# Kernel optimization log

Measured on AMD Instinct MI355X. Metric: run time of the kernel, lower is better.

## Reference

```python
import jax, jax.numpy as jnp
import numpy as np


def _gcn_norm(edge_index, num_nodes, dtype):
    # PyG GCNConv.norm: add self-loops (weight 1), symmetric deg^{-1/2} normalization
    row, col = edge_index[0], edge_index[1]
    loop = jnp.arange(num_nodes, dtype=row.dtype)
    row = jnp.concatenate([row, loop])
    col = jnp.concatenate([col, loop])
    ew = jnp.ones(row.shape[0], dtype=dtype)
    deg = jax.ops.segment_sum(ew, row, num_segments=num_nodes)
    dis = jnp.where(deg > 0, jax.lax.rsqrt(deg), 0.0)
    norm = dis[row] * ew * dis[col]
    return row, col, norm


def _masked_gcn_conv(x, row, col, norm, sigma, W, b, num_nodes):
    # mask_features: edge gather -> diff/sigma -> square -> scatter-add -> exp mask
    h = (x[col] - x[row]) / sigma            # [E, F]
    h = norm[:, None] * h * h                # [E, F]
    mask = jax.ops.segment_sum(h, row, num_segments=num_nodes)        # [N, F]
    deg = jax.ops.segment_sum(jnp.ones_like(norm), row, num_segments=num_nodes)  # degree(source), >=1 due to self-loops
    x = x * jnp.exp(-mask / deg[:, None])
    # GCNConv: linear transform then normalized aggregation source->target
    xw = x @ W                               # [N, O]
    out = jax.ops.segment_sum(norm[:, None] * xw[row], col, num_segments=num_nodes)
    return out + b


def setup_inputs() -> dict:
    key = jax.random.key(0)
    ks = jax.random.split(key, 8)
    N, E, F, H, C = 100000, 1600000, 128, 64, 40
    g = 1.414  # xavier gain used for sigma
    return {
        "x": jax.random.normal(ks[0], (N, F), jnp.float32),
        "edge_index": jax.random.randint(ks[1], (2, E), 0, N, jnp.int64),
        "sigma1": jax.random.uniform(ks[2], (1, F), jnp.float32, -1.0, 1.0) * (g * np.sqrt(6.0 / (1 + F))),
        "W1": jax.random.normal(ks[3], (F, H), jnp.float32) * (1.0 / np.sqrt(F)),
        "b1": jnp.zeros((H,), jnp.float32),
        "sigma2": jax.random.uniform(ks[4], (1, H), jnp.float32, -1.0, 1.0) * (g * np.sqrt(6.0 / (1 + H))),
        "W2": jax.random.normal(ks[5], (H, C), jnp.float32) * (1.0 / np.sqrt(H)),
        "b2": jnp.zeros((C,), jnp.float32),
    }


def reference(x, edge_index, sigma1, W1, b1, sigma2, W2, b2):
    N = x.shape[0]
    row, col, norm = _gcn_norm(edge_index, N, x.dtype)
    x = _masked_gcn_conv(x, row, col, norm, sigma1, W1, b1, N)
    x = jax.nn.relu(x)
    # dropout is identity in eval mode
    x = _masked_gcn_conv(x, row, col, norm, sigma2, W2, b2, N)
    return jax.nn.log_softmax(x, axis=1)
```

## Files before the change

kernel.cpp:

```cpp
#include <hip/hip_runtime.h>
#include <cmath>

constexpr int F1 = 128;
constexpr int H  = 64;
constexpr int NC = 40;
constexpr int NPART = 4;

constexpr int SCAN_TPB = 256;
constexpr int SCAN_IPT = 8;
constexpr int SCAN_EPB = SCAN_TPB * SCAN_IPT;

__device__ inline unsigned short f2bf(float f) {
    union { float f; unsigned u; } v; v.f = f;
    return (unsigned short)((v.u + 0x7FFFu + ((v.u >> 16) & 1u)) >> 16);
}
__device__ inline float bflo(unsigned p) { union { float f; unsigned u; } v; v.u = p << 16; return v.f; }
__device__ inline float bfhi(unsigned p) { union { float f; unsigned u; } v; v.u = p & 0xFFFF0000u; return v.f; }
__device__ inline void unpack8(uint4 raw, float* d) {
    d[0] = bflo(raw.x); d[1] = bfhi(raw.x); d[2] = bflo(raw.y); d[3] = bfhi(raw.y);
    d[4] = bflo(raw.z); d[5] = bfhi(raw.z); d[6] = bflo(raw.w); d[7] = bfhi(raw.w);
}

__global__ void isg_kernel(const float* __restrict__ s1, float* __restrict__ i1,
                           const float* __restrict__ s2, float* __restrict__ i2) {
    int i = threadIdx.x;
    if (i < F1) i1[i] = 1.0f / s1[i];
    if (i < H)  i2[i] = 1.0f / s2[i];
}

__global__ void count8_prep_kernel(const int* __restrict__ row, const int* __restrict__ col,
                                   int* __restrict__ cntO, int* __restrict__ cntI,
                                   int E, int chunk, int stride, int cntBlocks,
                                   const float* __restrict__ x, const float* __restrict__ isg,
                                   unsigned short* __restrict__ u, size_t n8) {
    int bid = blockIdx.x;
    if (bid < cntBlocks) {
        int p = bid & (NPART - 1);
        int gid = bid / NPART;
        unsigned lo = (unsigned)(p * chunk);
        for (int e = gid * blockDim.x + threadIdx.x; e < E; e += stride) {
            int r = row[e], c = col[e];
            if ((unsigned)r - lo < (unsigned)chunk) atomicAdd(&cntO[r], 1);
            if ((unsigned)c - lo < (unsigned)chunk) atomicAdd(&cntI[c], 1);
        }
    } else {
        size_t idx = (size_t)(bid - cntBlocks) * blockDim.x + threadIdx.x;
        if (idx >= n8) return;
        size_t base = idx * 8;
        int fk = (int)(base % (size_t)F1);
        float4 a0 = *(const float4*)&x[base];
        float4 a1 = *(const float4*)&x[base + 4];
        float4 s0 = *(const float4*)&isg[fk];
        float4 s1 = *(const float4*)&isg[fk + 4];
        uint4 p4;
        p4.x = (unsigned)f2bf(a0.x * s0.x) | ((unsigned)f2bf(a0.y * s0.y) << 16);
        p4.y = (unsigned)f2bf(a0.z * s0.z) | ((unsigned)f2bf(a0.w * s0.w) << 16);
        p4.z = (unsigned)f2bf(a1.x * s1.x) | ((unsigned)f2bf(a1.y * s1.y) << 16);
        p4.w = (unsigned)f2bf(a1.z * s1.z) | ((unsigned)f2bf(a1.w * s1.w) << 16);
        *(uint4*)&u[base] = p4;
    }
}

__global__ void scan_partial_kernel(const int* __restrict__ cnt, int* __restrict__ bsum, int M) {
    __shared__ int red[SCAN_TPB];
    int t = threadIdx.x;
    int i0 = blockIdx.x * SCAN_EPB + t * SCAN_IPT;
    int s = 0;
#pragma unroll
    for (int k = 0; k < SCAN_IPT; ++k) {
        int i = i0 + k;
        if (i < M) s += cnt[i];
    }
    red[t] = s;
    __syncthreads();
    for (int off = SCAN_TPB / 2; off > 0; off >>= 1) {
        if (t < off) red[t] += red[t + off];
        __syncthreads();
    }
    if (t == 0) bsum[blockIdx.x] = red[0];
}

__global__ void scan_offsets_kernel(int* __restrict__ bsum, int nb,
                                    int* __restrict__ rowptrO, int* __restrict__ rowptrI,
                                    int N, int E) {
    __shared__ int sh[1024];
    int t = threadIdx.x;
    sh[t] = (t < nb) ? bsum[t] : 0;
    __syncthreads();
    for (int off = 1; off < 1024; off <<= 1) {
        int v = (t >= off) ? sh[t - off] : 0;
        __syncthreads();
        sh[t] += v;
        __syncthreads();
    }
    if (t < nb) bsum[t] = (t > 0) ? sh[t - 1] : 0;
    if (t == 0) { rowptrO[N] = E; rowptrI[N] = E; }
}

__global__ void scan_final_kernel(int* __restrict__ cntO, int* __restrict__ cntI,
                                  const int* __restrict__ bsum,
                                  int* __restrict__ rowptrO, int* __restrict__ rowptrI,
                                  float* __restrict__ dis, int N, int E) {
    __shared__ int sh[SCAN_TPB];
    int t = threadIdx.x;
    int M = 2 * N;
    const int* cnt = cntO;
    int i0 = blockIdx.x * SCAN_EPB + t * SCAN_IPT;
    int cv[SCAN_IPT], pre[SCAN_IPT];
    int run = 0;
#pragma unroll
    for (int k = 0; k < SCAN_IPT; ++k) {
        int i = i0 + k;
        cv[k] = (i < M) ? cnt[i] : 0;
        pre[k] = run;
        run += cv[k];
    }
    sh[t] = run;
    __syncthreads();
    for (int off = 1; off < SCAN_TPB; off <<= 1) {
        int v = (t >= off) ? sh[t - off] : 0;
        __syncthreads();
        sh[t] += v;
        __syncthreads();
    }
    int toff = ((t > 0) ? sh[t - 1] : 0) + bsum[blockIdx.x];
#pragma unroll
    for (int k = 0; k < SCAN_IPT; ++k) {
        int i = i0 + k;
        if (i < M) {
            int val = toff + pre[k];
            if (i < N) {
                rowptrO[i] = val;
                cntO[i] = val;
                dis[i] = rsqrtf((float)(cv[k] + 1));
            } else {
                rowptrI[i - N] = val - E;
                cntI[i - N] = val - E;
            }
        }
    }
}

__global__ void build8_kernel(const int* __restrict__ row, const int* __restrict__ col,
                              int* __restrict__ curO, int* __restrict__ curI,
                              int2* __restrict__ adjO2, int2* __restrict__ adjI2,
                              const float* __restrict__ dis,
                              int E, int chunk, int stride) {
    int p = blockIdx.x & (NPART - 1);
    int gid = blockIdx.x / NPART;
    unsigned lo = (unsigned)(p * chunk);
    for (int e = gid * blockDim.x + threadIdx.x; e < E; e += stride) {
        int r = row[e], c = col[e];
        bool inR = (unsigned)r - lo < (unsigned)chunk;
        bool inC = (unsigned)c - lo < (unsigned)chunk;
        if (inR | inC) {
            float nrm = dis[r] * dis[c];
            int nb = __float_as_int(nrm);
            if (inR) adjO2[atomicAdd(&curO[r], 1)] = make_int2(c, nb);
            if (inC) adjI2[atomicAdd(&curI[c], 1)] = make_int2(r, nb);
        }
    }
}

template<int F, int O, int R>
__global__ void fused_mask_gemm_kernel(const int* __restrict__ rowptr, const int2* __restrict__ adj2,
                                       const float* __restrict__ sig,
                                       const unsigned short* __restrict__ u,
                                       const float* __restrict__ W,
                                       unsigned short* __restrict__ Ybf, int N) {
    constexpr int NT = R * 64;
    constexpr int G = F / 8;
    constexpr int NPI = 64 / G;
    __shared__ __align__(16) float Ws[F * O];
    __shared__ __align__(16) float Xs[R][F];
    int tid = threadIdx.x;
    for (int i = tid; i < F * O; i += NT) Ws[i] = W[i];
    int w = tid >> 6, lane = tid & 63;
    int h = lane / G, j = lane % G;
    int r = blockIdx.x * R + w;
    if (r < N) {
        int beg = rowptr[r], end = rowptr[r + 1];
        float inv_deg = 1.0f / (float)(end - beg + 1);
        float ur[8], acc[8];
        unpack8(*(const uint4*)&u[(size_t)r * F + 8 * j], ur);
#pragma unroll
        for (int k = 0; k < 8; ++k) acc[k] = 0.0f;
        for (int t = beg; t < end; t += 2 * NPI) {
            int e0 = t + h, e1 = t + NPI + h;
            int2 a0 = adj2[min(e0, end - 1)];
            int2 a1 = adj2[min(e1, end - 1)];
            float n0 = (e0 < end) ? __int_as_float(a0.y) : 0.0f;
            float n1 = (e1 < end) ? __int_as_float(a1.y) : 0.0f;
            uint4 rw0 = *(const uint4*)&u[(size_t)a0.x * F + 8 * j];
            uint4 rw1 = *(const uint4*)&u[(size_t)a1.x * F + 8 * j];
            float uc[8];
            unpack8(rw0, uc);
#pragma unroll
            for (int q = 0; q < 8; ++q) {
                float d = uc[q] - ur[q];
                acc[q] = fmaf(n0 * d, d, acc[q]);
            }
            unpack8(rw1, uc);
#pragma unroll
            for (int q = 0; q < 8; ++q) {
                float d = uc[q] - ur[q];
                acc[q] = fmaf(n1 * d, d, acc[q]);
            }
        }
#pragma unroll
        for (int off = G; off < 64; off <<= 1) {
#pragma unroll
            for (int k = 0; k < 8; ++k) acc[k] += __shfl_xor(acc[k], off);
        }
        if (h == 0) {
            float4 s0 = *(const float4*)&sig[8 * j];
            float4 s1 = *(const float4*)&sig[8 * j + 4];
            float sg[8] = {s0.x, s0.y, s0.z, s0.w, s1.x, s1.y, s1.z, s1.w};
            float xm[8];
#pragma unroll
            for (int k = 0; k < 8; ++k) xm[k] = ur[k] * sg[k] * expf(-acc[k] * inv_deg);
            *(float4*)&Xs[w][8 * j]     = make_float4(xm[0], xm[1], xm[2], xm[3]);
            *(float4*)&Xs[w][8 * j + 4] = make_float4(xm[4], xm[5], xm[6], xm[7]);
        }
    }
    __syncthreads();
    if (r < N && lane < O) {
        float acc = 0.0f;
#pragma unroll
        for (int fq = 0; fq < F / 4; ++fq) {
            float4 xs = *(const float4*)&Xs[w][4 * fq];
            acc = fmaf(xs.x, Ws[(4 * fq + 0) * O + lane], acc);
            acc = fmaf(xs.y, Ws[(4 * fq + 1) * O + lane], acc);
            acc = fmaf(xs.z, Ws[(4 * fq + 2) * O + lane], acc);
            acc = fmaf(xs.w, Ws[(4 * fq + 3) * O + lane], acc);
        }
        float other = __shfl_xor(acc, 1);
        if (!(lane & 1)) {
            *(unsigned*)&Ybf[(size_t)r * O + lane] =
                (unsigned)f2bf(acc) | ((unsigned)f2bf(other) << 16);
        }
    }
}

__global__ void agg_relu_kernel(const int* __restrict__ rowptr, const int2* __restrict__ adj2,
                                const float* __restrict__ dis, const unsigned short* __restrict__ ybf,
                                const float* __restrict__ bias,
                                unsigned short* __restrict__ u2, const float* __restrict__ isg2, int N) {
    int c = blockIdx.x * (blockDim.x >> 6) + (threadIdx.x >> 6);
    if (c >= N) return;
    int lane = threadIdx.x & 63;
    int h = lane >> 3, j = lane & 7;
    int beg = rowptr[c], end = rowptr[c + 1];
    float acc[8];
#pragma unroll
    for (int k = 0; k < 8; ++k) acc[k] = 0.0f;
    for (int t = beg; t < end; t += 16) {
        int e0 = t + h, e1 = t + 8 + h;
        int2 a0 = adj2[min(e0, end - 1)];
        int2 a1 = adj2[min(e1, end - 1)];
        float n0 = (e0 < end) ? __int_as_float(a0.y) : 0.0f;
        float n1 = (e1 < end) ? __int_as_float(a1.y) : 0.0f;
        uint4 rw0 = *(const uint4*)&ybf[(size_t)a0.x * H + 8 * j];
        uint4 rw1 = *(const uint4*)&ybf[(size_t)a1.x * H + 8 * j];
        float v[8];
        unpack8(rw0, v);
#pragma unroll
        for (int q = 0; q < 8; ++q) acc[q] = fmaf(n0, v[q], acc[q]);
        unpack8(rw1, v);
#pragma unroll
        for (int q = 0; q < 8; ++q) acc[q] = fmaf(n1, v[q], acc[q]);
    }
#pragma unroll
    for (int off = 8; off < 64; off <<= 1) {
#pragma unroll
        for (int k = 0; k < 8; ++k) acc[k] += __shfl_xor(acc[k], off);
    }
    if (h == 0) {
        float dc = dis[c];
        float sv[8];
        unpack8(*(const uint4*)&ybf[(size_t)c * H + 8 * j], sv);
        float4 b0 = *(const float4*)&bias[8 * j];
        float4 b1v = *(const float4*)&bias[8 * j + 4];
        float bb[8] = {b0.x, b0.y, b0.z, b0.w, b1v.x, b1v.y, b1v.z, b1v.w};
        float4 s0 = *(const float4*)&isg2[8 * j];
        float4 s1 = *(const float4*)&isg2[8 * j + 4];
        float sg[8] = {s0.x, s0.y, s0.z, s0.w, s1.x, s1.y, s1.z, s1.w};
        float hv[8];
        float d2 = dc * dc;
#pragma unroll
        for (int k = 0; k < 8; ++k) hv[k] = fmaxf(fmaf(d2, sv[k], acc[k]) + bb[k], 0.0f);
        uint4 p;
        p.x = (unsigned)f2bf(hv[0] * sg[0]) | ((unsigned)f2bf(hv[1] * sg[1]) << 16);
        p.y = (unsigned)f2bf(hv[2] * sg[2]) | ((unsigned)f2bf(hv[3] * sg[3]) << 16);
        p.z = (unsigned)f2bf(hv[4] * sg[4]) | ((unsigned)f2bf(hv[5] * sg[5]) << 16);
        p.w = (unsigned)f2bf(hv[6] * sg[6]) | ((unsigned)f2bf(hv[7] * sg[7]) << 16);
        *(uint4*)&u2[(size_t)c * H + 8 * j] = p;
    }
}

__global__ void agg_lsm_kernel(const int* __restrict__ rowptr, const int2* __restrict__ adj2,
                               const float* __restrict__ dis, const unsigned short* __restrict__ ybf,
                               const float* __restrict__ bias, float* __restrict__ out, int N) {
    int c = blockIdx.x * (blockDim.x >> 6) + (threadIdx.x >> 6);
    if (c >= N) return;
    int lane = threadIdx.x & 63;
    int h = lane >> 4, j = lane & 15;
    bool active = j < 10;
    int beg = rowptr[c], end = rowptr[c + 1];
    float a[4] = {0.f, 0.f, 0.f, 0.f};
    for (int t = beg; t < end; t += 8) {
        int e0 = t + h, e1 = t + 4 + h;
        int2 a0 = adj2[min(e0, end - 1)];
        int2 a1 = adj2[min(e1, end - 1)];
        float n0 = (e0 < end) ? __int_as_float(a0.y) : 0.0f;
        float n1 = (e1 < end) ? __int_as_float(a1.y) : 0.0f;
        uint2 rw0 = active ? *(const uint2*)&ybf[(size_t)a0.x * NC + 4 * j] : make_uint2(0u, 0u);
        uint2 rw1 = active ? *(const uint2*)&ybf[(size_t)a1.x * NC + 4 * j] : make_uint2(0u, 0u);
        a[0] = fmaf(n0, bflo(rw0.x), a[0]); a[1] = fmaf(n0, bfhi(rw0.x), a[1]);
        a[2] = fmaf(n0, bflo(rw0.y), a[2]); a[3] = fmaf(n0, bfhi(rw0.y), a[3]);
        a[0] = fmaf(n1, bflo(rw1.x), a[0]); a[1] = fmaf(n1, bfhi(rw1.x), a[1]);
        a[2] = fmaf(n1, bflo(rw1.y), a[2]); a[3] = fmaf(n1, bfhi(rw1.y), a[3]);
    }
#pragma unroll
    for (int off = 16; off < 64; off <<= 1) {
#pragma unroll
        for (int k = 0; k < 4; ++k) a[k] += __shfl_xor(a[k], off);
    }
    bool wr = (h == 0) && active;
    float v[4] = {-INFINITY, -INFINITY, -INFINITY, -INFINITY};
    if (wr) {
        float dc = dis[c];
        uint2 sr = *(const uint2*)&ybf[(size_t)c * NC + 4 * j];
        float sv[4] = {bflo(sr.x), bfhi(sr.x), bflo(sr.y), bfhi(sr.y)};
        float4 bb = *(const float4*)&bias[4 * j];
        float b4[4] = {bb.x, bb.y, bb.z, bb.w};
        float d2 = dc * dc;
#pragma unroll
        for (int k = 0; k < 4; ++k) v[k] = fmaf(d2, sv[k], a[k]) + b4[k];
    }
    float m = fmaxf(fmaxf(v[0], v[1]), fmaxf(v[2], v[3]));
#pragma unroll
    for (int off = 8; off > 0; off >>= 1) m = fmaxf(m, __shfl_xor(m, off));
    float s = wr ? (expf(v[0] - m) + expf(v[1] - m) + expf(v[2] - m) + expf(v[3] - m)) : 0.0f;
#pragma unroll
    for (int off = 8; off > 0; off >>= 1) s += __shfl_xor(s, off);
    float mls = m + logf(s);
    if (wr)
        *(float4*)&out[(size_t)c * NC + 4 * j] = make_float4(v[0] - mls, v[1] - mls, v[2] - mls, v[3] - mls);
}

extern "C" void kernel_launch(void* const* d_in, const int* in_sizes, int n_in,
                              void* d_out, int out_size, void* d_ws, size_t ws_size,
                              hipStream_t stream) {
    const float* x    = (const float*)d_in[0];
    const int*   ei   = (const int*)  d_in[1];
    const float* sig1 = (const float*)d_in[2];
    const float* W1   = (const float*)d_in[3];
    const float* b1   = (const float*)d_in[4];
    const float* sig2 = (const float*)d_in[5];
    const float* W2   = (const float*)d_in[6];
    const float* b2   = (const float*)d_in[7];
    float* out = (float*)d_out;

    const int N = in_sizes[0] / F1;
    const int E = in_sizes[1] / 2;
    const int* row = ei;
    const int* col = ei + E;

    char* w = (char*)d_ws;
    auto alloc = [&](size_t bytes) { void* q = w; w += (bytes + 255) & ~255ull; return q; };
    int*   cntO    = (int*)  alloc((size_t)2 * N * 4);
    int*   cntI    = cntO + N;
    int*   rowptrO = (int*)  alloc((size_t)(N + 1) * 4);
    int*   rowptrI = (int*)  alloc((size_t)(N + 1) * 4);
    int2*  adjO2   = (int2*) alloc((size_t)E * 8);
    int2*  adjI2   = (int2*) alloc((size_t)E * 8);
    float* dis     = (float*)alloc((size_t)N * 4);
    float* isg1    = (float*)alloc(F1 * 4);
    float* isg2    = (float*)alloc(H * 4);
    int*   bsum    = (int*)  alloc(1024 * 4);
    unsigned short* u1   = (unsigned short*)alloc((size_t)N * F1 * 2);
    unsigned short* u2   = (unsigned short*)alloc((size_t)N * H * 2);
    unsigned short* ybf1 = (unsigned short*)alloc((size_t)N * H * 2);
    unsigned short* ybf2 = u1;

    const int B = 256;
    const int chunk = (N + NPART - 1) / NPART;
    const int TOTB = 8192;
    const int stride4 = (TOTB / NPART) * B;
    const size_t n8 = (size_t)N * F1 / 8;
    const int prepBlocks = (int)((n8 + B - 1) / B);
    const int M = 2 * N;
    const int nb = (M + SCAN_EPB - 1) / SCAN_EPB;

    hipMemsetAsync(cntO, 0, (size_t)2 * N * 4, stream);
    isg_kernel<<<1, 128, 0, stream>>>(sig1, isg1, sig2, isg2);
    count8_prep_kernel<<<TOTB + prepBlocks, B, 0, stream>>>(
        row, col, cntO, cntI, E, chunk, stride4, TOTB, x, isg1, u1, n8);
    scan_partial_kernel<<<nb, SCAN_TPB, 0, stream>>>(cntO, bsum, M);
    scan_offsets_kernel<<<1, 1024, 0, stream>>>(bsum, nb, rowptrO, rowptrI, N, E);
    scan_final_kernel<<<nb, SCAN_TPB, 0, stream>>>(cntO, cntI, bsum, rowptrO, rowptrI, dis, N, E);
    build8_kernel<<<TOTB, B, 0, stream>>>(row, col, cntO, cntI, adjO2, adjI2, dis, E, chunk, stride4);

    fused_mask_gemm_kernel<F1, H, 8><<<(N + 7) / 8, 512, 0, stream>>>(rowptrO, adjO2, sig1, u1, W1, ybf1, N);
    agg_relu_kernel<<<(N + 3) / 4, B, 0, stream>>>(rowptrI, adjI2, dis, ybf1, b1, u2, isg2, N);

    fused_mask_gemm_kernel<H, NC, 8><<<(N + 7) / 8, 512, 0, stream>>>(rowptrO, adjO2, sig2, u2, W2, ybf2, N);
    agg_lsm_kernel<<<(N + 3) / 4, B, 0, stream>>>(rowptrI, adjI2, dis, ybf2, b2, out, N);
}
```

Before: 614.0 us.

## Split fused mask+GEMM into separate mask and bf16 GEMM kernels

Replaces the fused mask-then-GEMM kernel with two kernels. The mask kernel writes masked features to a bf16 buffer. A separate GEMM kernel then amortizes the shared-memory weight load over 64 rows per block instead of 8. The mask kernel now runs without the large shared-memory footprint, which should raise occupancy for the latency-bound gather. The cost is an extra global write and read of the intermediate, one more launch, and extra bf16 rounding of the masked features. Workspace buffers are re-aliased to hold the new intermediates.

After: 656.2 us. 1.07x slower.

```diff
diff --git a/kernel.cpp b/kernel.cpp
--- a/kernel.cpp
+++ b/kernel.cpp
@@ -162,83 +162,94 @@
     }
 }
 
-template<int F, int O, int R>
-__global__ void fused_mask_gemm_kernel(const int* __restrict__ rowptr, const int2* __restrict__ adj2,
-                                       const float* __restrict__ sig,
-                                       const unsigned short* __restrict__ u,
-                                       const float* __restrict__ W,
-                                       unsigned short* __restrict__ Ybf, int N) {
-    constexpr int NT = R * 64;
+template<int F>
+__global__ void mask_kernel(const int* __restrict__ rowptr, const int2* __restrict__ adj2,
+                            const float* __restrict__ sig,
+                            const unsigned short* __restrict__ u,
+                            unsigned short* __restrict__ xm, int N) {
     constexpr int G = F / 8;
     constexpr int NPI = 64 / G;
-    __shared__ __align__(16) float Ws[F * O];
-    __shared__ __align__(16) float Xs[R][F];
+    int w = threadIdx.x >> 6, lane = threadIdx.x & 63;
+    int h = lane / G, j = lane % G;
+    int r = blockIdx.x * (blockDim.x >> 6) + w;
+    if (r >= N) return;
+    int beg = rowptr[r], end = rowptr[r + 1];
+    float inv_deg = 1.0f / (float)(end - beg + 1);
+    float ur[8], acc[8];
+    unpack8(*(const uint4*)&u[(size_t)r * F + 8 * j], ur);
+#pragma unroll
+    for (int k = 0; k < 8; ++k) acc[k] = 0.0f;
+    for (int t = beg; t < end; t += 2 * NPI) {
+        int e0 = t + h, e1 = t + NPI + h;
+        int2 a0 = adj2[min(e0, end - 1)];
+        int2 a1 = adj2[min(e1, end - 1)];
+        float n0 = (e0 < end) ? __int_as_float(a0.y) : 0.0f;
+        float n1 = (e1 < end) ? __int_as_float(a1.y) : 0.0f;
+        uint4 rw0 = *(const uint4*)&u[(size_t)a0.x * F + 8 * j];
+        uint4 rw1 = *(const uint4*)&u[(size_t)a1.x * F + 8 * j];
+        float uc[8];
+        unpack8(rw0, uc);
+#pragma unroll
+        for (int q = 0; q < 8; ++q) {
+            float d = uc[q] - ur[q];
+            acc[q] = fmaf(n0 * d, d, acc[q]);
+        }
+        unpack8(rw1, uc);
+#pragma unroll
+        for (int q = 0; q < 8; ++q) {
+            float d = uc[q] - ur[q];
+            acc[q] = fmaf(n1 * d, d, acc[q]);
+        }
+    }
+#pragma unroll
+    for (int off = G; off < 64; off <<= 1) {
+#pragma unroll
+        for (int k = 0; k < 8; ++k) acc[k] += __shfl_xor(acc[k], off);
+    }
+    if (h == 0) {
+        float4 s0 = *(const float4*)&sig[8 * j];
+        float4 s1 = *(const float4*)&sig[8 * j + 4];
+        float sg[8] = {s0.x, s0.y, s0.z, s0.w, s1.x, s1.y, s1.z, s1.w};
+        float v[8];
+#pragma unroll
+        for (int k = 0; k < 8; ++k) v[k] = ur[k] * sg[k] * expf(-acc[k] * inv_deg);
+        uint4 p;
+        p.x = (unsigned)f2bf(v[0]) | ((unsigned)f2bf(v[1]) << 16);
+        p.y = (unsigned)f2bf(v[2]) | ((unsigned)f2bf(v[3]) << 16);
+        p.z = (unsigned)f2bf(v[4]) | ((unsigned)f2bf(v[5]) << 16);
+        p.w = (unsigned)f2bf(v[6]) | ((unsigned)f2bf(v[7]) << 16);
+        *(uint4*)&xm[(size_t)r * F + 8 * j] = p;
+    }
+}
+
+template<int F, int O>
+__global__ void gemm_bf_kernel(const unsigned short* __restrict__ xm, const float* __restrict__ W,
+                               unsigned short* __restrict__ ybf, int N) {
+    __shared__ float Ws[F * O];
     int tid = threadIdx.x;
-    for (int i = tid; i < F * O; i += NT) Ws[i] = W[i];
+    for (int i = tid; i < F * O; i += 256) Ws[i] = W[i];
+    __syncthreads();
     int w = tid >> 6, lane = tid & 63;
-    int h = lane / G, j = lane % G;
-    int r = blockIdx.x * R + w;
-    if (r < N) {
-        int beg = rowptr[r], end = rowptr[r + 1];
-        float inv_deg = 1.0f / (float)(end - beg + 1);
-        float ur[8], acc[8];
-        unpack8(*(const uint4*)&u[(size_t)r * F + 8 * j], ur);
-#pragma unroll
-        for (int k = 0; k < 8; ++k) acc[k] = 0.0f;
-        for (int t = beg; t < end; t += 2 * NPI) {
-            int e0 = t + h, e1 = t + NPI + h;
-            int2 a0 = adj2[min(e0, end - 1)];
-            int2 a1 = adj2[min(e1, end - 1)];
-            float n0 = (e0 < end) ? __int_as_float(a0.y) : 0.0f;
-            float n1 = (e1 < end) ? __int_as_float(a1.y) : 0.0f;
-            uint4 rw0 = *(const uint4*)&u[(size_t)a0.x * F + 8 * j];
-            uint4 rw1 = *(const uint4*)&u[(size_t)a1.x * F + 8 * j];
-            float uc[8];
-            unpack8(rw0, uc);
-#pragma unroll
-            for (int q = 0; q < 8; ++q) {
-                float d = uc[q] - ur[q];
-                acc[q] = fmaf(n0 * d, d, acc[q]);
-            }
-            unpack8(rw1, uc);
-#pragma unroll
-            for (int q = 0; q < 8; ++q) {
-                float d = uc[q] - ur[q];
-                acc[q] = fmaf(n1 * d, d, acc[q]);
-            }
-        }
-#pragma unroll
-        for (int off = G; off < 64; off <<= 1) {
-#pragma unroll
-            for (int k = 0; k < 8; ++k) acc[k] += __shfl_xor(acc[k], off);
-        }
-        if (h == 0) {
-            float4 s0 = *(const float4*)&sig[8 * j];
-            float4 s1 = *(const float4*)&sig[8 * j + 4];
-            float sg[8] = {s0.x, s0.y, s0.z, s0.w, s1.x, s1.y, s1.z, s1.w};
-            float xm[8];
-#pragma unroll
-            for (int k = 0; k < 8; ++k) xm[k] = ur[k] * sg[k] * expf(-acc[k] * inv_deg);
-            *(float4*)&Xs[w][8 * j]     = make_float4(xm[0], xm[1], xm[2], xm[3]);
-            *(float4*)&Xs[w][8 * j + 4] = make_float4(xm[4], xm[5], xm[6], xm[7]);
-        }
-    }
-    __syncthreads();
-    if (r < N && lane < O) {
+    if (lane >= O) return;
+    int r0 = blockIdx.x * 64 + w * 16;
+    for (int rr = 0; rr < 16; ++rr) {
+        int r = r0 + rr;
+        if (r >= N) break;
+        const unsigned short* xr = &xm[(size_t)r * F];
         float acc = 0.0f;
 #pragma unroll
-        for (int fq = 0; fq < F / 4; ++fq) {
-            float4 xs = *(const float4*)&Xs[w][4 * fq];
-            acc = fmaf(xs.x, Ws[(4 * fq + 0) * O + lane], acc);
-            acc = fmaf(xs.y, Ws[(4 * fq + 1) * O + lane], acc);
-            acc = fmaf(xs.z, Ws[(4 * fq + 2) * O + lane], acc);
-            acc = fmaf(xs.w, Ws[(4 * fq + 3) * O + lane], acc);
+        for (int fq = 0; fq < F / 8; ++fq) {
+            uint4 raw = *(const uint4*)&xr[8 * fq];
+            float xv[8];
+            unpack8(raw, xv);
+#pragma unroll
+            for (int k = 0; k < 8; ++k)
+                acc = fmaf(xv[k], Ws[(8 * fq + k) * O + lane], acc);
         }
         float other = __shfl_xor(acc, 1);
-        if (!(lane & 1)) {
-            *(unsigned*)&Ybf[(size_t)r * O + lane] =
+        if (!(lane & 1))
+            *(unsigned*)&ybf[(size_t)r * O + lane] =
                 (unsigned)f2bf(acc) | ((unsigned)f2bf(other) << 16);
-        }
     }
 }
 
@@ -379,10 +390,14 @@
     float* isg1    = (float*)alloc(F1 * 4);
     float* isg2    = (float*)alloc(H * 4);
     int*   bsum    = (int*)  alloc(1024 * 4);
-    unsigned short* u1   = (unsigned short*)alloc((size_t)N * F1 * 2);
+    unsigned short* regA = (unsigned short*)alloc((size_t)N * F1 * 2);
+    unsigned short* regB = (unsigned short*)alloc((size_t)N * F1 * 2);
     unsigned short* u2   = (unsigned short*)alloc((size_t)N * H * 2);
-    unsigned short* ybf1 = (unsigned short*)alloc((size_t)N * H * 2);
-    unsigned short* ybf2 = u1;
+    unsigned short* u1   = regA;
+    unsigned short* ybf1 = regA;
+    unsigned short* xm2  = regA + (size_t)N * H;
+    unsigned short* xm1  = regB;
+    unsigned short* ybf2 = regB;
 
     const int B = 256;
     const int chunk = (N + NPART - 1) / NPART;
@@ -402,9 +417,11 @@
     scan_final_kernel<<<nb, SCAN_TPB, 0, stream>>>(cntO, cntI, bsum, rowptrO, rowptrI, dis, N, E);
     build8_kernel<<<TOTB, B, 0, stream>>>(row, col, cntO, cntI, adjO2, adjI2, dis, E, chunk, stride4);
 
-    fused_mask_gemm_kernel<F1, H, 8><<<(N + 7) / 8, 512, 0, stream>>>(rowptrO, adjO2, sig1, u1, W1, ybf1, N);
+    mask_kernel<F1><<<(N + 3) / 4, B, 0, stream>>>(rowptrO, adjO2, sig1, u1, xm1, N);
+    gemm_bf_kernel<F1, H><<<(N + 63) / 64, B, 0, stream>>>(xm1, W1, ybf1, N);
     agg_relu_kernel<<<(N + 3) / 4, B, 0, stream>>>(rowptrI, adjI2, dis, ybf1, b1, u2, isg2, N);
 
-    fused_mask_gemm_kernel<H, NC, 8><<<(N + 7) / 8, 512, 0, stream>>>(rowptrO, adjO2, sig2, u2, W2, ybf2, N);
+    mask_kernel<H><<<(N + 3) / 4, B, 0, stream>>>(rowptrO, adjO2, sig2, u2, xm2, N);
+    gemm_bf_kernel<H, NC><<<(N + 63) / 64, B, 0, stream>>>(xm2, W2, ybf2, N);
     agg_lsm_kernel<<<(N + 3) / 4, B, 0, stream>>>(rowptrI, adjI2, dis, ybf2, b2, out, N);
 }
```
